# Performance work log

Hardware: AMD Instinct MI355X
Metric: run time of the kernel (lower is better)

The kernel has to match this reference:

```python
import jax, jax.numpy as jnp
import numpy as np
import math

EMBED_DIM = 1024
NUM_HEADS = 16
D_K = EMBED_DIM // NUM_HEADS
B, S = 2, 2048


def setup_inputs() -> dict:
    key = jax.random.key(0)
    ks = jax.random.split(key, 6)
    scale = 1.0 / math.sqrt(EMBED_DIM)
    x = jax.random.normal(ks[0], (B, S, EMBED_DIM), dtype=jnp.float32)
    mask = jax.random.randint(ks[1], (B, S), 0, 2) > 0  # True = masked-out key
    wq = jax.random.normal(ks[2], (EMBED_DIM, EMBED_DIM), dtype=jnp.float32) * scale
    wk = jax.random.normal(ks[3], (EMBED_DIM, EMBED_DIM), dtype=jnp.float32) * scale
    wv = jax.random.normal(ks[4], (EMBED_DIM, EMBED_DIM), dtype=jnp.float32) * scale
    wo = jax.random.normal(ks[5], (EMBED_DIM, EMBED_DIM), dtype=jnp.float32) * scale
    return {"x": x, "mask": mask, "wq": wq, "wk": wk, "wv": wv, "wo": wo}


def reference(x, mask, wq, wk, wv, wo):
    b, s, _ = x.shape
    # torch nn.Linear(bias=False): y = x @ W.T
    q = (x @ wq.T).reshape(b, s, NUM_HEADS, D_K).transpose(0, 2, 1, 3)  # [B,H,S,Dk]
    k = (x @ wk.T).reshape(b, s, NUM_HEADS, D_K).transpose(0, 2, 1, 3)
    v = (x @ wv.T).reshape(b, s, NUM_HEADS, D_K).transpose(0, 2, 1, 3)
    scores = jnp.einsum('bhqd,bhkd->bhqk', q, k) / math.sqrt(D_K)
    # mask [B,S] -> [B,1,1,S]: key-padding mask, True filled with -1e9
    scores = jnp.where(mask[:, None, None, :], jnp.float32(-1e9), scores)
    attn = jax.nn.softmax(scores, axis=-1)
    # dropout in eval mode -> identity
    out = jnp.einsum('bhqk,bhkd->bhqd', attn, v)
    out = out.transpose(0, 2, 1, 3).reshape(b, s, EMBED_DIM)
    return out @ wo.T
```

## Files before the change

kernel.cpp:

```cpp
#include <hip/hip_runtime.h>
#include <hip/hip_bf16.h>


typedef unsigned short u16;
typedef unsigned int u32;
using short8 = __attribute__((ext_vector_type(8))) short;
using f32x4  = __attribute__((ext_vector_type(4))) float;

#define WS_XB    0u
#define WS_WQKV  8388608u
#define WS_WOB   14680064u
#define WS_QB    16777216u
#define WS_KB    25165824u
#define WS_VTB   33554432u
#define WS_OB    41943040u

__device__ __forceinline__ u16 f2bf(float f) {
  u32 u = __float_as_uint(f);
  u += 0x7fffu + ((u >> 16) & 1u);
  return (u16)(u >> 16);
}

__device__ __forceinline__ ushort4 pk4(f32x4 v) {
  ushort4 r; r.x = f2bf(v[0]); r.y = f2bf(v[1]); r.z = f2bf(v[2]); r.w = f2bf(v[3]);
  return r;
}

__device__ __forceinline__ u32 pkbf2(float lo, float hi) {
  union { __hip_bfloat162 b; u32 u; } c;
  c.b = __float22bfloat162_rn(make_float2(lo, hi));
  return c.u;
}

__device__ __forceinline__ void gload16(const void* g, void* l) {
  __builtin_amdgcn_global_load_lds(
      (const __attribute__((address_space(1))) u32*)g,
      (__attribute__((address_space(3))) u32*)l, 16, 0, 0);
}

#define KSCALE 0.18033688011112042f

__global__ void convert_k(const float* __restrict__ x, const float* __restrict__ wq,
                          const float* __restrict__ wk, const float* __restrict__ wv,
                          const float* __restrict__ wo,
                          u16* __restrict__ xb, u16* __restrict__ wqkv, u16* __restrict__ wob) {
  size_t g = ((size_t)blockIdx.x * 256 + threadIdx.x) * 4;
  const float* s; u16* d;
  if (g < 4194304u)      { s = x  + g;            d = xb   + g; }
  else if (g < 5242880u) { s = wq + (g - 4194304u); d = wqkv + (g - 4194304u); }
  else if (g < 6291456u) { s = wk + (g - 5242880u); d = wqkv + 1048576u + (g - 5242880u); }
  else if (g < 7340032u) { s = wv + (g - 6291456u); d = wqkv + 2097152u + (g - 6291456u); }
  else                   { s = wo + (g - 7340032u); d = wob  + (g - 7340032u); }
  float4 v = *(const float4*)s;
  f32x4 vv = {v.x, v.y, v.z, v.w};
  *(ushort4*)d = pk4(vv);
}

__global__ void gemm_qkv(const u16* __restrict__ A, const u16* __restrict__ Bt,
                         u16* __restrict__ qb, u16* __restrict__ kb, u16* __restrict__ vtb) {
  __shared__ __align__(16) u16 As[128 * 64];
  __shared__ __align__(16) u16 Bs[128 * 64];
  const int tid  = threadIdx.x;
  const int wave = tid >> 6, lane = tid & 63;
  const int c16  = lane & 15, quad = lane >> 4;
  const int tile_m = blockIdx.x * 128;
  const int tile_n = blockIdx.y * 128;
  const int wm = (wave >> 1) * 64, wn = (wave & 1) * 64;
  const int srow = wave * 32 + (lane >> 3);
  const int sc   = lane & 7;
  const int which = blockIdx.y >> 3;
  const bool swp  = (which < 2);

  const u16* Pa = swp ? Bs : As;
  const u16* Pb = swp ? As : Bs;
  const int  ra = swp ? wn : wm;
  const int  rb = swp ? wm : wn;

  f32x4 acc[4][4] = {};

  for (int k0 = 0; k0 < 1024; k0 += 64) {
    __syncthreads();
#pragma unroll
    for (int j = 0; j < 4; ++j) {
      int row = srow + j * 8;
      int cp  = sc ^ (row & 7);
      gload16(A  + (size_t)(tile_m + row) * 1024 + k0 + cp * 8, As + row * 64 + sc * 8);
      gload16(Bt + (size_t)(tile_n + row) * 1024 + k0 + cp * 8, Bs + row * 64 + sc * 8);
    }
    __syncthreads();
#pragma unroll
    for (int kc = 0; kc < 2; ++kc) {
      const int ch = ((kc * 4 + quad) ^ (c16 & 7)) * 8;
      short8 fa[4], fb[4];
#pragma unroll
      for (int i = 0; i < 4; ++i)
        fa[i] = *(const short8*)(Pa + (ra + i * 16 + c16) * 64 + ch);
#pragma unroll
      for (int j = 0; j < 4; ++j)
        fb[j] = *(const short8*)(Pb + (rb + j * 16 + c16) * 64 + ch);
#pragma unroll
      for (int i = 0; i < 4; ++i)
#pragma unroll
        for (int j = 0; j < 4; ++j)
          acc[i][j] = __builtin_amdgcn_mfma_f32_16x16x32_bf16(fa[i], fb[j], acc[i][j], 0, 0, 0);
    }
  }

  if (which == 2) {
#pragma unroll
    for (int i = 0; i < 4; ++i) {
      int m0 = tile_m + wm + i * 16 + quad * 4;
      int bb = m0 >> 11, ss0 = m0 & 2047;
#pragma unroll
      for (int j = 0; j < 4; ++j) {
        int f = (tile_n & 1023) + wn + j * 16 + c16;
        int h = f >> 6, d = f & 63;
        *(ushort4*)(vtb + ((size_t)(bb * 16 + h) * 64 + d) * 2048 + ss0) = pk4(acc[i][j]);
      }
    }
  } else {
    u16* dstb = which ? kb : qb;
#pragma unroll
    for (int i = 0; i < 4; ++i) {
      int full = (tile_n & 1023) + wn + i * 16 + quad * 4;
      int h = full >> 6, d0 = full & 63;
#pragma unroll
      for (int j = 0; j < 4; ++j) {
        int t = tile_m + wm + j * 16 + c16;
        int bb = t >> 11, ss = t & 2047;
        f32x4 v = acc[i][j];
        if (which == 0) { v[0] *= KSCALE; v[1] *= KSCALE; v[2] *= KSCALE; v[3] *= KSCALE; }
        *(ushort4*)(dstb + ((size_t)(bb * 16 + h) * 2048 + ss) * 64 + d0) = pk4(v);
      }
    }
  }
}

__global__ __launch_bounds__(512) void attn_k(const u16* __restrict__ qb, const u16* __restrict__ kb,
                                              const u16* __restrict__ vtb, const int* __restrict__ mask,
                                              u16* __restrict__ ob) {
  __shared__ __align__(16) char smem[53248];
  u16* const KsB   = (u16*)smem;
  u16* const VsB   = (u16*)(smem + 16384);
  u16* const Ps    = (u16*)(smem + 32768);
  u32* const mask2 = (u32*)(smem + 49152);

  const int tid  = threadIdx.x;
  const int wave = tid >> 6, lane = tid & 63;
  const int c16  = lane & 15, g4 = lane >> 4;
  const int qg   = wave >> 1;
  const int kh   = wave & 1;

  const int f    = blockIdx.x + 16 * blockIdx.y;
  const int i64  = f >> 3;
  const int bh   = (f & 7) * 4 + (i64 >> 4);
  const int q0   = (i64 & 15) * 128;
  const int bidx = bh >> 4, h = bh & 15;

  {
    int4 m0 = *(const int4*)(mask + bidx * 2048 + tid * 4);
    uint2 dd;
    dd.x = (m0.x ? 0u : 0xFFFFu) | (m0.y ? 0u : 0xFFFF0000u);
    dd.y = (m0.z ? 0u : 0xFFFFu) | (m0.w ? 0u : 0xFFFF0000u);
    *(uint2*)(mask2 + tid * 2) = dd;
  }

  const u16* qg_ = qb + ((size_t)bh * 2048 + q0 + qg * 32) * 64;
  short8 qf[2][2];
#pragma unroll
  for (int kc = 0; kc < 2; ++kc)
#pragma unroll
    for (int nj = 0; nj < 2; ++nj)
      qf[kc][nj] = *(const short8*)(qg_ + (nj * 16 + c16) * 64 + kc * 32 + g4 * 8);

  const u16* kg = kb  + (size_t)bh * 2048 * 64;
  const u16* vg = vtb + (size_t)bh * 64 * 2048;
  {
    int r  = tid >> 3;
    int cp = (tid & 7) ^ (r & 7);
    gload16(kg + (size_t)r * 64 + cp * 8,   KsB + tid * 8);
    gload16(vg + (size_t)r * 2048 + cp * 8, VsB + tid * 8);
  }
  __syncthreads();

  short8 ones;
#pragma unroll
  for (int i = 0; i < 8; ++i) ones[i] = (short)0x3F80;

  f32x4 O[2][4] = {};
  f32x4 L[2] = {};

#pragma unroll 2
  for (int kt = 0; kt < 32; ++kt) {
    if (kt) __syncthreads();
    if (kt + 1 < 32) {
      const int nb = (kt + 1) & 1;
      int r  = tid >> 3;
      int cp = (tid & 7) ^ (r & 7);
      gload16(kg + (size_t)((kt + 1) * 64 + r) * 64 + cp * 8, KsB + nb * 4096 + tid * 8);
      gload16(vg + (size_t)r * 2048 + (kt + 1) * 64 + cp * 8, VsB + nb * 4096 + tid * 8);
    }
    const u16* ksb = KsB + (kt & 1) * 4096;
    const u16* vsb = VsB + (kt & 1) * 4096;

    f32x4 S[2][2] = {};
    __builtin_amdgcn_s_setprio(1);
#pragma unroll
    for (int kc = 0; kc < 2; ++kc) {
      const int ch = ((kc * 4 + g4) ^ (c16 & 7)) * 8;
      short8 a[2];
#pragma unroll
      for (int mi = 0; mi < 2; ++mi)
        a[mi] = *(const short8*)(ksb + (kh * 32 + mi * 16 + c16) * 64 + ch);
#pragma unroll
      for (int mi = 0; mi < 2; ++mi)
#pragma unroll
        for (int nj = 0; nj < 2; ++nj)
          S[mi][nj] = __builtin_amdgcn_mfma_f32_16x16x32_bf16(a[mi], qf[kc][nj], S[mi][nj], 0, 0, 0);
    }
    __builtin_amdgcn_s_setprio(0);

    uint2 mk[2];
#pragma unroll
    for (int mi = 0; mi < 2; ++mi)
      mk[mi] = *(const uint2*)(mask2 + kt * 32 + kh * 16 + mi * 8 + g4 * 2);

#pragma unroll
    for (int nj = 0; nj < 2; ++nj) {
      const int q = qg * 32 + nj * 16 + c16;
#pragma unroll
      for (int mi = 0; mi < 2; ++mi) {
        float p0 = __builtin_amdgcn_exp2f(S[mi][nj][0]);
        float p1 = __builtin_amdgcn_exp2f(S[mi][nj][1]);
        float p2 = __builtin_amdgcn_exp2f(S[mi][nj][2]);
        float p3 = __builtin_amdgcn_exp2f(S[mi][nj][3]);
        u32 lo = pkbf2(p0, p1) & mk[mi].x;
        u32 hi = pkbf2(p2, p3) & mk[mi].y;
        uint2 pkd; pkd.x = lo; pkd.y = hi;
        const int c = kh * 4 + mi * 2 + (g4 >> 1);
        *(uint2*)(Ps + q * 64 + ((c ^ (c16 & 7)) * 8 + (g4 & 1) * 4)) = pkd;
      }
    }

    {
      const int ch = ((kh * 4 + g4) ^ (c16 & 7)) * 8;
      short8 a2[2], b2[4];
#pragma unroll
      for (int mi = 0; mi < 2; ++mi)
        a2[mi] = *(const short8*)(Ps + (qg * 32 + mi * 16 + c16) * 64 + ch);
#pragma unroll
      for (int nd = 0; nd < 4; ++nd)
        b2[nd] = *(const short8*)(vsb + (nd * 16 + c16) * 64 + ch);
      __builtin_amdgcn_s_setprio(1);
#pragma unroll
      for (int mi = 0; mi < 2; ++mi) {
#pragma unroll
        for (int nd = 0; nd < 4; ++nd)
          O[mi][nd] = __builtin_amdgcn_mfma_f32_16x16x32_bf16(a2[mi], b2[nd], O[mi][nd], 0, 0, 0);
        L[mi] = __builtin_amdgcn_mfma_f32_16x16x32_bf16(a2[mi], ones, L[mi], 0, 0, 0);
      }
      __builtin_amdgcn_s_setprio(0);
    }
  }

  __syncthreads();
  float* const redO = (float*)smem;
  float* const redL = (float*)(smem + 33792);
  if (kh) {
#pragma unroll
    for (int mi = 0; mi < 2; ++mi)
#pragma unroll
      for (int r = 0; r < 4; ++r) {
        int row = qg * 32 + mi * 16 + g4 * 4 + r;
#pragma unroll
        for (int nd = 0; nd < 4; ++nd)
          redO[row * 66 + nd * 16 + c16] = O[mi][nd][r];
        if (c16 == 0) redL[row] = L[mi][r];
      }
  }
  __syncthreads();
  if (!kh) {
    u16* og = ob + ((size_t)(bidx * 2048 + q0 + qg * 32)) * 1024 + h * 64;
#pragma unroll
    for (int mi = 0; mi < 2; ++mi)
#pragma unroll
      for (int r = 0; r < 4; ++r) {
        int row  = qg * 32 + mi * 16 + g4 * 4 + r;
        int qrow = mi * 16 + g4 * 4 + r;
        float linv = 1.f / (L[mi][r] + redL[row]);
#pragma unroll
        for (int nd = 0; nd < 4; ++nd) {
          float o = O[mi][nd][r] + redO[row * 66 + nd * 16 + c16];
          og[(size_t)qrow * 1024 + nd * 16 + c16] = f2bf(o * linv);
        }
      }
  }
}

__global__ __launch_bounds__(256) void gemm_out(const u16* __restrict__ A, const u16* __restrict__ Bt,
                         float* __restrict__ out) {
  __shared__ __align__(16) u16 As[128 * 64];
  __shared__ __align__(16) u16 Bs[64 * 64];
  const int tid  = threadIdx.x;
  const int wave = tid >> 6, lane = tid & 63;
  const int c16  = lane & 15, quad = lane >> 4;
  const int tile_m = blockIdx.x * 128;
  const int tile_n = blockIdx.y * 64;
  const int wm = wave * 32;
  const int sc   = lane & 7;

  f32x4 acc[4][2] = {};

  for (int k0 = 0; k0 < 1024; k0 += 64) {
    __syncthreads();
#pragma unroll
    for (int j = 0; j < 4; ++j) {
      int row = (tid >> 3) + j * 32;
      int cp  = sc ^ (row & 7);
      gload16(A + (size_t)(tile_m + row) * 1024 + k0 + cp * 8, As + row * 64 + sc * 8);
    }
#pragma unroll
    for (int j = 0; j < 2; ++j) {
      int row = (tid >> 3) + j * 32;
      int cp  = sc ^ (row & 7);
      gload16(Bt + (size_t)(tile_n + row) * 1024 + k0 + cp * 8, Bs + row * 64 + sc * 8);
    }
    __syncthreads();
#pragma unroll
    for (int kc = 0; kc < 2; ++kc) {
      const int ch = ((kc * 4 + quad) ^ (c16 & 7)) * 8;
      short8 fa[4], fb[2];
#pragma unroll
      for (int i = 0; i < 4; ++i)
        fa[i] = *(const short8*)(Bs + (i * 16 + c16) * 64 + ch);
#pragma unroll
      for (int j = 0; j < 2; ++j)
        fb[j] = *(const short8*)(As + (wm + j * 16 + c16) * 64 + ch);
#pragma unroll
      for (int i = 0; i < 4; ++i)
#pragma unroll
        for (int j = 0; j < 2; ++j)
          acc[i][j] = __builtin_amdgcn_mfma_f32_16x16x32_bf16(fa[i], fb[j], acc[i][j], 0, 0, 0);
    }
  }
#pragma unroll
  for (int i = 0; i < 4; ++i) {
    int f0 = tile_n + i * 16 + quad * 4;
#pragma unroll
    for (int j = 0; j < 2; ++j) {
      int t = tile_m + wm + j * 16 + c16;
      *(f32x4*)(out + (size_t)t * 1024 + f0) = acc[i][j];
    }
  }
}

extern "C" void kernel_launch(void* const* d_in, const int* in_sizes, int n_in,
                              void* d_out, int out_size, void* d_ws, size_t ws_size,
                              hipStream_t stream) {
  (void)in_sizes; (void)n_in; (void)out_size; (void)ws_size;
  const float* x    = (const float*)d_in[0];
  const int*   mask = (const int*)d_in[1];
  const float* wq   = (const float*)d_in[2];
  const float* wk   = (const float*)d_in[3];
  const float* wv   = (const float*)d_in[4];
  const float* wo   = (const float*)d_in[5];
  float* out = (float*)d_out;
  char*  ws  = (char*)d_ws;

  u16* xb   = (u16*)(ws + WS_XB);
  u16* wqkv = (u16*)(ws + WS_WQKV);
  u16* wob  = (u16*)(ws + WS_WOB);
  u16* qbuf = (u16*)(ws + WS_QB);
  u16* kbuf = (u16*)(ws + WS_KB);
  u16* vtb  = (u16*)(ws + WS_VTB);
  u16* obuf = (u16*)(ws + WS_OB);

  convert_k<<<8192, 256, 0, stream>>>(x, wq, wk, wv, wo, xb, wqkv, wob);
  gemm_qkv<<<dim3(32, 24), 256, 0, stream>>>(xb, wqkv, qbuf, kbuf, vtb);
  attn_k<<<dim3(16, 32), 512, 0, stream>>>(qbuf, kbuf, vtb, mask, obuf);
  gemm_out<<<dim3(32, 16), 256, 0, stream>>>(obuf, wob, out);
}
```

Before: 179.7 us.

## Software-pipeline attention loop: overlap previous tile's PV MFMAs with current QK

Restructures the attention inner loop so the P·V and row-sum MFMAs for tile kt-1 are issued alongside the Q·K MFMAs for tile kt, with an epilogue for the last tile. To support this, P is double-buffered and V is triple-buffered in LDS, and K fragments are preloaded into registers before the MFMA block. The aim is to hide the exp/pack/LDS-store latency between the two matmuls and let the MFMA pipe stay busy. The cost is LDS growing from 52 KB to 76 KB per block, which can lower the number of resident blocks per CU. The explicit unroll-by-2 pragma is also dropped.

```diff
diff --git a/kernel.cpp b/kernel.cpp
--- a/kernel.cpp
+++ b/kernel.cpp
@@ -139,11 +139,11 @@
 __global__ __launch_bounds__(512) void attn_k(const u16* __restrict__ qb, const u16* __restrict__ kb,
                                               const u16* __restrict__ vtb, const int* __restrict__ mask,
                                               u16* __restrict__ ob) {
-  __shared__ __align__(16) char smem[53248];
+  __shared__ __align__(16) char smem[77824];
   u16* const KsB   = (u16*)smem;
   u16* const VsB   = (u16*)(smem + 16384);
-  u16* const Ps    = (u16*)(smem + 32768);
-  u32* const mask2 = (u32*)(smem + 49152);
+  u16* const PsB   = (u16*)(smem + 40960);
+  u32* const mask2 = (u32*)(smem + 73728);
 
   const int tid  = threadIdx.x;
   const int wave = tid >> 6, lane = tid & 63;
@@ -190,41 +190,66 @@
   f32x4 O[2][4] = {};
   f32x4 L[2] = {};
 
-#pragma unroll 2
   for (int kt = 0; kt < 32; ++kt) {
     if (kt) __syncthreads();
     if (kt + 1 < 32) {
-      const int nb = (kt + 1) & 1;
       int r  = tid >> 3;
       int cp = (tid & 7) ^ (r & 7);
-      gload16(kg + (size_t)((kt + 1) * 64 + r) * 64 + cp * 8, KsB + nb * 4096 + tid * 8);
-      gload16(vg + (size_t)r * 2048 + (kt + 1) * 64 + cp * 8, VsB + nb * 4096 + tid * 8);
-    }
-    const u16* ksb = KsB + (kt & 1) * 4096;
-    const u16* vsb = VsB + (kt & 1) * 4096;
+      gload16(kg + (size_t)((kt + 1) * 64 + r) * 64 + cp * 8,
+              KsB + ((kt + 1) & 1) * 4096 + tid * 8);
+      gload16(vg + (size_t)r * 2048 + (kt + 1) * 64 + cp * 8,
+              VsB + ((kt + 1) % 3) * 4096 + tid * 8);
+    }
+
+    short8 a2[2], b2[4];
+    if (kt) {
+      const u16* psb = PsB + ((kt - 1) & 1) * 8192;
+      const u16* vsb = VsB + ((kt - 1) % 3) * 4096;
+      const int ch = ((kh * 4 + g4) ^ (c16 & 7)) * 8;
+#pragma unroll
+      for (int mi = 0; mi < 2; ++mi)
+        a2[mi] = *(const short8*)(psb + (qg * 32 + mi * 16 + c16) * 64 + ch);
+#pragma unroll
+      for (int nd = 0; nd < 4; ++nd)
+        b2[nd] = *(const short8*)(vsb + (nd * 16 + c16) * 64 + ch);
+    }
+    short8 ka[2][2];
+    {
+      const u16* ksb = KsB + (kt & 1) * 4096;
+#pragma unroll
+      for (int kc = 0; kc < 2; ++kc) {
+        const int ch = ((kc * 4 + g4) ^ (c16 & 7)) * 8;
+#pragma unroll
+        for (int mi = 0; mi < 2; ++mi)
+          ka[kc][mi] = *(const short8*)(ksb + (kh * 32 + mi * 16 + c16) * 64 + ch);
+      }
+    }
 
     f32x4 S[2][2] = {};
     __builtin_amdgcn_s_setprio(1);
-#pragma unroll
-    for (int kc = 0; kc < 2; ++kc) {
-      const int ch = ((kc * 4 + g4) ^ (c16 & 7)) * 8;
-      short8 a[2];
+    if (kt) {
+#pragma unroll
+      for (int mi = 0; mi < 2; ++mi) {
+#pragma unroll
+        for (int nd = 0; nd < 4; ++nd)
+          O[mi][nd] = __builtin_amdgcn_mfma_f32_16x16x32_bf16(a2[mi], b2[nd], O[mi][nd], 0, 0, 0);
+        L[mi] = __builtin_amdgcn_mfma_f32_16x16x32_bf16(a2[mi], ones, L[mi], 0, 0, 0);
+      }
+    }
+#pragma unroll
+    for (int kc = 0; kc < 2; ++kc)
 #pragma unroll
       for (int mi = 0; mi < 2; ++mi)
-        a[mi] = *(const short8*)(ksb + (kh * 32 + mi * 16 + c16) * 64 + ch);
-#pragma unroll
-      for (int mi = 0; mi < 2; ++mi)
 #pragma unroll
         for (int nj = 0; nj < 2; ++nj)
-          S[mi][nj] = __builtin_amdgcn_mfma_f32_16x16x32_bf16(a[mi], qf[kc][nj], S[mi][nj], 0, 0, 0);
-    }
+          S[mi][nj] = __builtin_amdgcn_mfma_f32_16x16x32_bf16(ka[kc][mi], qf[kc][nj], S[mi][nj], 0, 0, 0);
     __builtin_amdgcn_s_setprio(0);
 
     uint2 mk[2];
 #pragma unroll
     for (int mi = 0; mi < 2; ++mi)
       mk[mi] = *(const uint2*)(mask2 + kt * 32 + kh * 16 + mi * 8 + g4 * 2);
-
+    u16* psw = PsB + (kt & 1) * 8192;
 #pragma unroll
     for (int nj = 0; nj < 2; ++nj) {
       const int q = qg * 32 + nj * 16 + c16;
@@ -238,28 +263,28 @@
         u32 hi = pkbf2(p2, p3) & mk[mi].y;
         uint2 pkd; pkd.x = lo; pkd.y = hi;
         const int c = kh * 4 + mi * 2 + (g4 >> 1);
-        *(uint2*)(Ps + q * 64 + ((c ^ (c16 & 7)) * 8 + (g4 & 1) * 4)) = pkd;
-      }
-    }
-
-    {
-      const int ch = ((kh * 4 + g4) ^ (c16 & 7)) * 8;
-      short8 a2[2], b2[4];
-#pragma unroll
-      for (int mi = 0; mi < 2; ++mi)
-        a2[mi] = *(const short8*)(Ps + (qg * 32 + mi * 16 + c16) * 64 + ch);
+        *(uint2*)(psw + q * 64 + ((c ^ (c16 & 7)) * 8 + (g4 & 1) * 4)) = pkd;
+      }
+    }
+  }
+
+  {
+    const u16* psb = PsB + 8192;
+    const u16* vsb = VsB + 4096;
+    const int ch = ((kh * 4 + g4) ^ (c16 & 7)) * 8;
+    short8 a2[2], b2[4];
+#pragma unroll
+    for (int mi = 0; mi < 2; ++mi)
+      a2[mi] = *(const short8*)(psb + (qg * 32 + mi * 16 + c16) * 64 + ch);
+#pragma unroll
+    for (int nd = 0; nd < 4; ++nd)
+      b2[nd] = *(const short8*)(vsb + (nd * 16 + c16) * 64 + ch);
+#pragma unroll
+    for (int mi = 0; mi < 2; ++mi) {
 #pragma unroll
       for (int nd = 0; nd < 4; ++nd)
-        b2[nd] = *(const short8*)(vsb + (nd * 16 + c16) * 64 + ch);
-      __builtin_amdgcn_s_setprio(1);
-#pragma unroll
-      for (int mi = 0; mi < 2; ++mi) {
-#pragma unroll
-        for (int nd = 0; nd < 4; ++nd)
-          O[mi][nd] = __builtin_amdgcn_mfma_f32_16x16x32_bf16(a2[mi], b2[nd], O[mi][nd], 0, 0, 0);
-        L[mi] = __builtin_amdgcn_mfma_f32_16x16x32_bf16(a2[mi], ones, L[mi], 0, 0, 0);
-      }
-      __builtin_amdgcn_s_setprio(0);
+        O[mi][nd] = __builtin_amdgcn_mfma_f32_16x16x32_bf16(a2[mi], b2[nd], O[mi][nd], 0, 0, 0);
+      L[mi] = __builtin_amdgcn_mfma_f32_16x16x32_bf16(a2[mi], ones, L[mi], 0, 0, 0);
     }
   }
 
```

Measured after the change: 185.7 us. 1.03x slower.

## Keep attention probabilities in registers using 32x32 MFMA and permlane swaps

Applied to the files above, without the earlier changes.

Reworks the attention kernel to use 32x32x16 bf16 MFMAs for both QK^T and PV. The probability tile no longer round-trips through shared memory; it is rearranged into the PV operand layout in registers with v_permlane32_swap. The row-sum is accumulated with scalar adds instead of an extra MFMA against a ones vector. This removes the Ps LDS writes and reads and the L MFMAs, and shrinks shared memory, at the cost of inline asm and a more intricate lane mapping whose correctness depends on the MFMA output layout.

```diff
diff --git a/kernel.cpp b/kernel.cpp
--- a/kernel.cpp
+++ b/kernel.cpp
@@ -6,6 +6,7 @@
 typedef unsigned int u32;
 using short8 = __attribute__((ext_vector_type(8))) short;
 using f32x4  = __attribute__((ext_vector_type(4))) float;
+using f32x16 = __attribute__((ext_vector_type(16))) float;
 
 #define WS_XB    0u
 #define WS_WQKV  8388608u
@@ -139,15 +140,14 @@
 __global__ __launch_bounds__(512) void attn_k(const u16* __restrict__ qb, const u16* __restrict__ kb,
                                               const u16* __restrict__ vtb, const int* __restrict__ mask,
                                               u16* __restrict__ ob) {
-  __shared__ __align__(16) char smem[53248];
+  __shared__ __align__(16) char smem[36864];
   u16* const KsB   = (u16*)smem;
   u16* const VsB   = (u16*)(smem + 16384);
-  u16* const Ps    = (u16*)(smem + 32768);
-  u32* const mask2 = (u32*)(smem + 49152);
+  u32* const mask2 = (u32*)(smem + 32768);
 
   const int tid  = threadIdx.x;
   const int wave = tid >> 6, lane = tid & 63;
-  const int c16  = lane & 15, g4 = lane >> 4;
+  const int q32  = lane & 31, hi = lane >> 5;
   const int qg   = wave >> 1;
   const int kh   = wave & 1;
 
@@ -166,12 +166,10 @@
   }
 
   const u16* qg_ = qb + ((size_t)bh * 2048 + q0 + qg * 32) * 64;
-  short8 qf[2][2];
-#pragma unroll
-  for (int kc = 0; kc < 2; ++kc)
-#pragma unroll
-    for (int nj = 0; nj < 2; ++nj)
-      qf[kc][nj] = *(const short8*)(qg_ + (nj * 16 + c16) * 64 + kc * 32 + g4 * 8);
+  short8 qf[4];
+#pragma unroll
+  for (int kc = 0; kc < 4; ++kc)
+    qf[kc] = *(const short8*)(qg_ + q32 * 64 + kc * 16 + hi * 8);
 
   const u16* kg = kb  + (size_t)bh * 2048 * 64;
   const u16* vg = vtb + (size_t)bh * 64 * 2048;
@@ -183,14 +181,11 @@
   }
   __syncthreads();
 
-  short8 ones;
-#pragma unroll
-  for (int i = 0; i < 8; ++i) ones[i] = (short)0x3F80;
-
-  f32x4 O[2][4] = {};
-  f32x4 L[2] = {};
-
-#pragma unroll 2
+  f32x16 O[2] = {};
+  float  Lv   = 0.f;
+
+  const int krow = kh * 32 + q32;
+
   for (int kt = 0; kt < 32; ++kt) {
     if (kt) __syncthreads();
     if (kt + 1 < 32) {
@@ -203,97 +198,111 @@
     const u16* ksb = KsB + (kt & 1) * 4096;
     const u16* vsb = VsB + (kt & 1) * 4096;
 
-    f32x4 S[2][2] = {};
+    short8 ka[4];
+#pragma unroll
+    for (int kc = 0; kc < 4; ++kc) {
+      const int c8 = (kc * 2 + hi) ^ (krow & 7);
+      ka[kc] = *(const short8*)(ksb + krow * 64 + c8 * 8);
+    }
+
+    f32x16 S = {};
     __builtin_amdgcn_s_setprio(1);
 #pragma unroll
-    for (int kc = 0; kc < 2; ++kc) {
-      const int ch = ((kc * 4 + g4) ^ (c16 & 7)) * 8;
-      short8 a[2];
-#pragma unroll
-      for (int mi = 0; mi < 2; ++mi)
-        a[mi] = *(const short8*)(ksb + (kh * 32 + mi * 16 + c16) * 64 + ch);
-#pragma unroll
-      for (int mi = 0; mi < 2; ++mi)
-#pragma unroll
-        for (int nj = 0; nj < 2; ++nj)
-          S[mi][nj] = __builtin_amdgcn_mfma_f32_16x16x32_bf16(a[mi], qf[kc][nj], S[mi][nj], 0, 0, 0);
-    }
+    for (int kc = 0; kc < 4; ++kc)
+      S = __builtin_amdgcn_mfma_f32_32x32x16_bf16(ka[kc], qf[kc], S, 0, 0, 0);
     __builtin_amdgcn_s_setprio(0);
 
-    uint2 mk[2];
-#pragma unroll
-    for (int mi = 0; mi < 2; ++mi)
-      mk[mi] = *(const uint2*)(mask2 + kt * 32 + kh * 16 + mi * 8 + g4 * 2);
-
-#pragma unroll
-    for (int nj = 0; nj < 2; ++nj) {
-      const int q = qg * 32 + nj * 16 + c16;
-#pragma unroll
-      for (int mi = 0; mi < 2; ++mi) {
-        float p0 = __builtin_amdgcn_exp2f(S[mi][nj][0]);
-        float p1 = __builtin_amdgcn_exp2f(S[mi][nj][1]);
-        float p2 = __builtin_amdgcn_exp2f(S[mi][nj][2]);
-        float p3 = __builtin_amdgcn_exp2f(S[mi][nj][3]);
-        u32 lo = pkbf2(p0, p1) & mk[mi].x;
-        u32 hi = pkbf2(p2, p3) & mk[mi].y;
-        uint2 pkd; pkd.x = lo; pkd.y = hi;
-        const int c = kh * 4 + mi * 2 + (g4 >> 1);
-        *(uint2*)(Ps + q * 64 + ((c ^ (c16 & 7)) * 8 + (g4 & 1) * 4)) = pkd;
+    u32 X[4][2];
+#pragma unroll
+    for (int g = 0; g < 4; ++g) {
+      uint2 mg = *(const uint2*)(mask2 + kt * 32 + kh * 16 + g * 4 + hi * 2);
+      float p0 = __builtin_amdgcn_exp2f(S[4 * g + 0]);
+      float p1 = __builtin_amdgcn_exp2f(S[4 * g + 1]);
+      float p2 = __builtin_amdgcn_exp2f(S[4 * g + 2]);
+      float p3 = __builtin_amdgcn_exp2f(S[4 * g + 3]);
+      u32 x0 = pkbf2(p0, p1) & mg.x;
+      u32 x1 = pkbf2(p2, p3) & mg.y;
+      Lv += __uint_as_float(x0 << 16) + __uint_as_float(x0 & 0xFFFF0000u)
+          + __uint_as_float(x1 << 16) + __uint_as_float(x1 & 0xFFFF0000u);
+      X[g][0] = x0; X[g][1] = x1;
+    }
+
+    short8 pa0, pa1;
+    {
+      u32 a0 = X[0][0], b0 = X[1][0];
+      asm("v_permlane32_swap_b32 %0, %1" : "+v"(a0), "+v"(b0));
+      u32 a1 = X[0][1], b1 = X[1][1];
+      asm("v_permlane32_swap_b32 %0, %1" : "+v"(a1), "+v"(b1));
+      union { u32 u[4]; short8 s; } pw;
+      pw.u[0] = a0; pw.u[1] = a1; pw.u[2] = b0; pw.u[3] = b1;
+      pa0 = pw.s;
+      u32 c0 = X[2][0], d0 = X[3][0];
+      asm("v_permlane32_swap_b32 %0, %1" : "+v"(c0), "+v"(d0));
+      u32 c1 = X[2][1], d1 = X[3][1];
+      asm("v_permlane32_swap_b32 %0, %1" : "+v"(c1), "+v"(d1));
+      union { u32 u[4]; short8 s; } pw2;
+      pw2.u[0] = c0; pw2.u[1] = c1; pw2.u[2] = d0; pw2.u[3] = d1;
+      pa1 = pw2.s;
+    }
+
+    short8 vb00, vb01, vb10, vb11;
+    {
+      const int r0 = q32, r1 = 32 + q32;
+      vb00 = *(const short8*)(vsb + r0 * 64 + (((kh * 4 + 0 * 2 + hi) ^ (r0 & 7)) * 8));
+      vb01 = *(const short8*)(vsb + r0 * 64 + (((kh * 4 + 1 * 2 + hi) ^ (r0 & 7)) * 8));
+      vb10 = *(const short8*)(vsb + r1 * 64 + (((kh * 4 + 0 * 2 + hi) ^ (r1 & 7)) * 8));
+      vb11 = *(const short8*)(vsb + r1 * 64 + (((kh * 4 + 1 * 2 + hi) ^ (r1 & 7)) * 8));
+    }
+    __builtin_amdgcn_s_setprio(1);
+    O[0] = __builtin_amdgcn_mfma_f32_32x32x16_bf16(pa0, vb00, O[0], 0, 0, 0);
+    O[0] = __builtin_amdgcn_mfma_f32_32x32x16_bf16(pa1, vb01, O[0], 0, 0, 0);
+    O[1] = __builtin_amdgcn_mfma_f32_32x32x16_bf16(pa0, vb10, O[1], 0, 0, 0);
+    O[1] = __builtin_amdgcn_mfma_f32_32x32x16_bf16(pa1, vb11, O[1], 0, 0, 0);
+    __builtin_amdgcn_s_setprio(0);
+  }
+
+  float Lw;
+  {
+    u32 la = __float_as_uint(Lv), lb = la;
+    asm("v_permlane32_swap_b32 %0, %1" : "+v"(la), "+v"(lb));
+    Lw = __uint_as_float(la) + __uint_as_float(lb);
+  }
+
+  __syncthreads();
+  float* const redO  = (float*)smem;
+  float* const redL0 = (float*)(smem + 33792);
+  float* const redL1 = (float*)(smem + 34304);
+  if (kh) {
+#pragma unroll
+    for (int qd = 0; qd < 4; ++qd)
+#pragma unroll
+      for (int t = 0; t < 4; ++t) {
+        const int r   = qd * 4 + t;
+        const int row = qg * 32 + qd * 8 + hi * 4 + t;
+        redO[row * 66 +      q32] = O[0][r];
+        redO[row * 66 + 32 + q32] = O[1][r];
       }
-    }
-
-    {
-      const int ch = ((kh * 4 + g4) ^ (c16 & 7)) * 8;
-      short8 a2[2], b2[4];
-#pragma unroll
-      for (int mi = 0; mi < 2; ++mi)
-        a2[mi] = *(const short8*)(Ps + (qg * 32 + mi * 16 + c16) * 64 + ch);
-#pragma unroll
-      for (int nd = 0; nd < 4; ++nd)
-        b2[nd] = *(const short8*)(vsb + (nd * 16 + c16) * 64 + ch);
-      __builtin_amdgcn_s_setprio(1);
-#pragma unroll
-      for (int mi = 0; mi < 2; ++mi) {
-#pragma unroll
-        for (int nd = 0; nd < 4; ++nd)
-          O[mi][nd] = __builtin_amdgcn_mfma_f32_16x16x32_bf16(a2[mi], b2[nd], O[mi][nd], 0, 0, 0);
-        L[mi] = __builtin_amdgcn_mfma_f32_16x16x32_bf16(a2[mi], ones, L[mi], 0, 0, 0);
-      }
-      __builtin_amdgcn_s_setprio(0);
-    }
-  }
-
-  __syncthreads();
-  float* const redO = (float*)smem;
-  float* const redL = (float*)(smem + 33792);
-  if (kh) {
-#pragma unroll
-    for (int mi = 0; mi < 2; ++mi)
-#pragma unroll
-      for (int r = 0; r < 4; ++r) {
-        int row = qg * 32 + mi * 16 + g4 * 4 + r;
-#pragma unroll
-        for (int nd = 0; nd < 4; ++nd)
-          redO[row * 66 + nd * 16 + c16] = O[mi][nd][r];
-        if (c16 == 0) redL[row] = L[mi][r];
-      }
+    if (lane < 32) redL1[qg * 32 + q32] = Lw;
+  } else {
+    if (lane < 32) redL0[qg * 32 + q32] = Lw;
   }
   __syncthreads();
   if (!kh) {
     u16* og = ob + ((size_t)(bidx * 2048 + q0 + qg * 32)) * 1024 + h * 64;
 #pragma unroll
-    for (int mi = 0; mi < 2; ++mi)
-#pragma unroll
-      for (int r = 0; r < 4; ++r) {
-        int row  = qg * 32 + mi * 16 + g4 * 4 + r;
-        int qrow = mi * 16 + g4 * 4 + r;
-        float linv = 1.f / (L[mi][r] + redL[row]);
-#pragma unroll
-        for (int nd = 0; nd < 4; ++nd) {
-          float o = O[mi][nd][r] + redO[row * 66 + nd * 16 + c16];
-          og[(size_t)qrow * 1024 + nd * 16 + c16] = f2bf(o * linv);
-        }
+    for (int qd = 0; qd < 4; ++qd) {
+      f32x4 l0 = *(const f32x4*)(redL0 + qg * 32 + qd * 8 + hi * 4);
+      f32x4 l1 = *(const f32x4*)(redL1 + qg * 32 + qd * 8 + hi * 4);
+#pragma unroll
+      for (int t = 0; t < 4; ++t) {
+        const int r    = qd * 4 + t;
+        const int crow = qd * 8 + hi * 4 + t;
+        const int row  = qg * 32 + crow;
+        const float linv = 1.f / (l0[t] + l1[t]);
+        og[(size_t)crow * 1024 +      q32] = f2bf((O[0][r] + redO[row * 66 +      q32]) * linv);
+        og[(size_t)crow * 1024 + 32 + q32] = f2bf((O[1][r] + redO[row * 66 + 32 + q32]) * linv);
       }
+    }
   }
 }
 
```

Result: slower. 184.1 us (+2.4%).
